# Kernel optimization log

Measured on AMD Instinct MI355X. Metric: run time of the kernel, lower is better.

## Reference

```python
import jax, jax.numpy as jnp
import numpy as np
import math

T, HW, M, D, DK, H, SIGMA = 16, 1024, 256, 768, 768, 8, 0.5
HD = DK // H
VHD = D // H
EPS = 1e-6
SCALE = 1.0 / math.sqrt(HD)


def _ln(x, g):
    # LayerNorm(eps=1e-6, bias=False)
    m = x.mean(-1, keepdims=True)
    v = ((x - m) ** 2).mean(-1, keepdims=True)
    return (x - m) / jnp.sqrt(v + EPS) * g


def setup_inputs() -> dict:
    key = jax.random.key(0)
    ks = jax.random.split(key, 16)
    s = 0.02
    features = jax.random.normal(ks[0], (T, HW, D), jnp.float32)
    tracks = jax.random.uniform(ks[1], (T, M, 2), jnp.float32)
    track_pos_embeddings = jax.random.normal(ks[2], (T, M, D), jnp.float32)
    feature_pos_embeddings = jax.random.normal(ks[3], (T, HW, D), jnp.float32)
    g = jnp.linspace(0.0, 1.0, 32)
    feature_positions = jnp.stack(jnp.meshgrid(g, g, indexing='ij'), axis=-1).reshape(HW, 2)
    return {
        'features': features,
        'tracks': tracks,
        'feature_positions': feature_positions,
        'track_pos_embeddings': track_pos_embeddings,
        'feature_pos_embeddings': feature_pos_embeddings,
        # AttentionalSampling params (nn.Linear weights are [out,in])
        'Wq_s': jax.random.normal(ks[4], (DK, D)) * s,
        'Wk_s': jax.random.normal(ks[5], (DK, D)) * s,
        'Wv_s': jax.random.normal(ks[6], (D, D)) * s,
        'qg_s': jnp.ones((DK,), jnp.float32),
        'kg_s': jnp.ones((DK,), jnp.float32),
        'Wo_s': jax.random.normal(ks[7], (D, D)) * s,
        # AttentionalSplatting params
        'Wq_p': jax.random.normal(ks[8], (DK, D)) * s,
        'Wk_p': jax.random.normal(ks[9], (DK, D)) * s,
        'Wv_p': jax.random.normal(ks[10], (D, D)) * s,
        'qg_p': jnp.ones((DK,), jnp.float32),
        'kg_p': jnp.ones((DK,), jnp.float32),
        'Wout_p': jax.random.normal(ks[11], (D, D)) * s,
    }


def reference(features, tracks, feature_positions, track_pos_embeddings,
              feature_pos_embeddings, Wq_s, Wk_s, Wv_s, qg_s, kg_s, Wo_s,
              Wq_p, Wk_p, Wv_p, qg_p, kg_p, Wout_p):
    # per-frame Gaussian spatial bias from squared euclidean distances
    # d2[t,m,n] = ||tracks[t,m] - feature_positions[n]||^2  -> [T, M, HW]
    d2 = ((tracks[:, :, None, :] - feature_positions[None, None, :, :]) ** 2).sum(-1)
    bias = -d2 / (2.0 * SIGMA ** 2)  # [T, M, HW]

    # ---- Attentional Sampling: tracks query features ----
    Q = _ln(track_pos_embeddings @ Wq_s.T, qg_s)          # [T, M, DK]
    K = _ln((features + feature_pos_embeddings) @ Wk_s.T, kg_s)  # [T, HW, DK]
    V = features @ Wv_s.T                                  # [T, HW, D]
    Qh = Q.reshape(T, M, H, HD).transpose(0, 2, 1, 3)      # [T, H, M, HD]
    Kh = K.reshape(T, HW, H, HD).transpose(0, 2, 1, 3)     # [T, H, HW, HD]
    Vh = V.reshape(T, HW, H, VHD).transpose(0, 2, 1, 3)    # [T, H, HW, VHD]
    scores = jnp.einsum('thmd,thnd->thmn', Qh, Kh) * SCALE + bias[:, None]
    A = jax.nn.softmax(scores, axis=-1)
    sampled = jnp.einsum('thmn,thnd->thmd', A, Vh)
    sampled = sampled.transpose(0, 2, 1, 3).reshape(T, M, D) @ Wo_s.T  # [T, M, D]

    # ---- Attentional Splatting: features query tracks ----
    Q2 = _ln(feature_pos_embeddings @ Wq_p.T, qg_p)        # [T, HW, DK]
    K2 = _ln(track_pos_embeddings @ Wk_p.T, kg_p)          # [T, M, DK]
    V2 = sampled @ Wv_p.T                                   # [T, M, D]
    Q2h = Q2.reshape(T, HW, H, HD).transpose(0, 2, 1, 3)   # [T, H, HW, HD]
    K2h = K2.reshape(T, M, H, HD).transpose(0, 2, 1, 3)    # [T, H, M, HD]
    V2h = V2.reshape(T, M, H, VHD).transpose(0, 2, 1, 3)   # [T, H, M, VHD]
    bias_t = jnp.swapaxes(bias, 1, 2)                       # [T, HW, M] (cdist is symmetric)
    scores2 = jnp.einsum('thnd,thmd->thnm', Q2h, K2h) * SCALE + bias_t[:, None]
    A2 = jax.nn.softmax(scores2, axis=-1)
    upd = jnp.einsum('thnm,thmd->thnd', A2, V2h)
    feature_updates = upd.transpose(0, 2, 1, 3).reshape(T, HW, D) @ Wout_p.T
    return features + feature_updates
```

## Files before the change

### kernel.cpp

```cpp
#include <hip/hip_runtime.h>

#define DD 768
#define HDIM 96
#define ATT_SCALE 0.10206207261596575f

typedef float floatx4 __attribute__((ext_vector_type(4)));
typedef __bf16 bf16;
typedef bf16 bf16x8 __attribute__((ext_vector_type(8)));
typedef bf16 bf16x4 __attribute__((ext_vector_type(4)));

__device__ __forceinline__ void gl2lds16(const bf16* g, bf16* l) {
  __builtin_amdgcn_global_load_lds(
      (const __attribute__((address_space(1))) void*)g,
      (__attribute__((address_space(3))) void*)l, 16, 0, 0);
}

__global__ __launch_bounds__(256) void conv_fuse(const float* __restrict__ f,
                                                 const float* __restrict__ e,
                                                 bf16* __restrict__ fb,
                                                 bf16* __restrict__ xb,
                                                 bf16* __restrict__ eb) {
  const int i = (blockIdx.x * 256 + threadIdx.x) * 8;
  floatx4 f0 = *(const floatx4*)(f + i);
  floatx4 f1 = *(const floatx4*)(f + i + 4);
  floatx4 e0 = *(const floatx4*)(e + i);
  floatx4 e1 = *(const floatx4*)(e + i + 4);
  bf16x8 fv, xv, ev;
#pragma unroll
  for (int k = 0; k < 4; k++) {
    fv[k] = (bf16)f0[k];           fv[k + 4] = (bf16)f1[k];
    ev[k] = (bf16)e0[k];           ev[k + 4] = (bf16)e1[k];
    xv[k] = (bf16)(f0[k] + e0[k]); xv[k + 4] = (bf16)(f1[k] + e1[k]);
  }
  *(bf16x8*)(fb + i) = fv;
  *(bf16x8*)(xb + i) = xv;
  *(bf16x8*)(eb + i) = ev;
}

__global__ __launch_bounds__(256) void f2b(const float* __restrict__ s,
                                           bf16* __restrict__ d) {
  const int i = (blockIdx.x * 256 + threadIdx.x) * 8;
  floatx4 s0 = *(const floatx4*)(s + i);
  floatx4 s1 = *(const floatx4*)(s + i + 4);
  bf16x8 v;
#pragma unroll
  for (int k = 0; k < 4; k++) { v[k] = (bf16)s0[k]; v[k + 4] = (bf16)s1[k]; }
  *(bf16x8*)(d + i) = v;
}

__global__ __launch_bounds__(256) void wconv(const float* w0, const float* w1,
                                             const float* w2, const float* w3,
                                             const float* w4, const float* w5,
                                             const float* w6, const float* w7,
                                             bf16* __restrict__ dst) {
  const float* srcs[8] = {w0, w1, w2, w3, w4, w5, w6, w7};
  const float* s = srcs[blockIdx.y];
  bf16* d = dst + (size_t)blockIdx.y * 589824;
  const int i = (blockIdx.x * 256 + threadIdx.x) * 8;
  floatx4 s0 = *(const floatx4*)(s + i);
  floatx4 s1 = *(const floatx4*)(s + i + 4);
  bf16x8 v;
#pragma unroll
  for (int k = 0; k < 4; k++) { v[k] = (bf16)s0[k]; v[k + 4] = (bf16)s1[k]; }
  *(bf16x8*)(d + i) = v;
}

__device__ __forceinline__ void ln_row(bf16* x, const float* g, int lane) {
  float v[12], s = 0.f, ss = 0.f;
#pragma unroll
  for (int j = 0; j < 3; j++) {
    bf16x4 b = *(const bf16x4*)&x[j * 256 + lane * 4];
#pragma unroll
    for (int e = 0; e < 4; e++) {
      float t = (float)b[e];
      v[j * 4 + e] = t; s += t; ss += t * t;
    }
  }
#pragma unroll
  for (int o = 32; o > 0; o >>= 1) { s += __shfl_xor(s, o); ss += __shfl_xor(ss, o); }
  const float mean = s * (1.0f / DD);
  const float inv = rsqrtf(ss * (1.0f / DD) - mean * mean + 1e-6f);
#pragma unroll
  for (int j = 0; j < 3; j++) {
    floatx4 gg = *(const floatx4*)&g[j * 256 + lane * 4];
    bf16x4 o4;
#pragma unroll
    for (int e = 0; e < 4; e++) o4[e] = (bf16)((v[j * 4 + e] - mean) * inv * gg[e]);
    *(bf16x4*)&x[j * 256 + lane * 4] = o4;
  }
}

__global__ __launch_bounds__(256) void ln_all(bf16* X0, const float* g0,
                                              bf16* X1, const float* g1,
                                              bf16* X2, const float* g2,
                                              bf16* X3, const float* g3) {
  const int b = blockIdx.x;
  bf16* X; const float* g; int base;
  if (b < 4096)      { X = X0; g = g0; base = b; }
  else if (b < 8192) { X = X1; g = g1; base = b - 4096; }
  else if (b < 9216) { X = X2; g = g2; base = b - 8192; }
  else               { X = X3; g = g3; base = b - 9216; }
  const int w = threadIdx.x >> 6, lane = threadIdx.x & 63;
  ln_row(X + (size_t)(base * 4 + w) * DD, g, lane);
}

template <int MODE>
__device__ __forceinline__ void gemm_core(const bf16* __restrict__ A,
                                          const bf16* __restrict__ W,
                                          bf16* __restrict__ Cb,
                                          float* __restrict__ Cf,
                                          const float* __restrict__ addsrc,
                                          bf16* As, bf16* Ws) {
  const int tid = threadIdx.x;
  const int lane = tid & 63;
  const int w = tid >> 6;
  const int row0 = blockIdx.x * 128;
  const int col0 = blockIdx.y * 128;
  const int wm = (w & 1) * 64;
  const int wn = (w >> 1) * 64;
  const int fr = lane & 15;
  const int quad = lane >> 4;
  const int srow = tid >> 2;
  const int scol = (tid & 3) * 8;
  const bf16* Ag = A + (size_t)(row0 + srow) * DD + scol;
  const bf16* Wg = W + (size_t)(col0 + srow) * DD + scol;
  bf16* AsD = &As[tid * 8];
  bf16* WsD = &Ws[tid * 8];

  floatx4 acc[4][4];
#pragma unroll
  for (int i = 0; i < 4; i++)
#pragma unroll
    for (int j = 0; j < 4; j++) acc[i][j] = (floatx4){0, 0, 0, 0};

  for (int k0 = 0; k0 < DD; k0 += 32) {
    __syncthreads();
    gl2lds16(Ag + k0, AsD);
    gl2lds16(Ag + k0 + (size_t)64 * DD, AsD + 2048);
    gl2lds16(Wg + k0, WsD);
    gl2lds16(Wg + k0 + (size_t)64 * DD, WsD + 2048);
    __syncthreads();
    bf16x8 af[4], bfr[4];
#pragma unroll
    for (int i = 0; i < 4; i++)
      af[i] = *(const bf16x8*)&As[(wm + i * 16 + fr) * 32 + quad * 8];
#pragma unroll
    for (int j = 0; j < 4; j++)
      bfr[j] = *(const bf16x8*)&Ws[(wn + j * 16 + fr) * 32 + quad * 8];
#pragma unroll
    for (int i = 0; i < 4; i++)
#pragma unroll
      for (int j = 0; j < 4; j++)
        acc[i][j] = __builtin_amdgcn_mfma_f32_16x16x32_bf16(af[i], bfr[j], acc[i][j], 0, 0, 0);
  }
#pragma unroll
  for (int i = 0; i < 4; i++)
#pragma unroll
    for (int j = 0; j < 4; j++)
#pragma unroll
      for (int r = 0; r < 4; r++) {
        const int row = row0 + wm + i * 16 + quad * 4 + r;
        const int col = col0 + wn + j * 16 + fr;
        const size_t idx = (size_t)row * DD + col;
        if (MODE == 0) Cb[idx] = (bf16)acc[i][j][r];
        else Cf[idx] = acc[i][j][r] + addsrc[idx];
      }
}

__global__ __launch_bounds__(256) void gemm_b(const bf16* A, const bf16* W, bf16* C) {
  __shared__ bf16 As[4096], Ws[4096];
  gemm_core<0>(A, W, C, nullptr, nullptr, As, Ws);
}

__global__ __launch_bounds__(256) void gemm_b2(const bf16* A0, const bf16* W0, bf16* C0,
                                               const bf16* A1, const bf16* W1, bf16* C1) {
  __shared__ bf16 As[4096], Ws[4096];
  if (blockIdx.z == 0) gemm_core<0>(A0, W0, C0, nullptr, nullptr, As, Ws);
  else                 gemm_core<0>(A1, W1, C1, nullptr, nullptr, As, Ws);
}

__global__ __launch_bounds__(256) void gemm_final(const bf16* A, const bf16* W,
                                                  float* C, const float* addsrc) {
  __shared__ bf16 As[4096], Ws[4096];
  gemm_core<1>(A, W, nullptr, C, addsrc, As, Ws);
}

template <int RPW, int SPLIT>
__global__ __launch_bounds__(256) void attn_kernel(
    const bf16* __restrict__ Qb, const bf16* __restrict__ Kb,
    const bf16* __restrict__ Vb, bf16* __restrict__ Ob,
    float* __restrict__ Ml,
    const float* __restrict__ qpos, int qpos_ts,
    const float* __restrict__ kpos, int kpos_ts,
    int nq, int nk, int nqt, int nsp) {
  const int b = blockIdx.x;
  const int h = b & 7;
  const int t = (b >> 3) & 15;
  const int rest = b >> 7;
  const int qt = rest % nqt;
  const int sp = rest / nqt;
  const int klen = nk / nsp;
  const int k0s = sp * klen;
  const int q0 = qt * (64 * RPW);
  const bf16* Q = Qb + (size_t)t * nq * DD + h * HDIM;
  const bf16* K = Kb + (size_t)t * nk * DD + h * HDIM;
  const bf16* V = Vb + (size_t)t * nk * DD + h * HDIM;
  bf16* O = Ob + (size_t)(SPLIT ? (sp * 16 + t) : t) * nq * DD + h * HDIM;
  const float* qp = qpos + (size_t)t * qpos_ts;
  const float* kp = kpos + (size_t)t * kpos_ts;

  __shared__ bf16 Ks[64 * 104];
  __shared__ bf16 Vt[96 * 72];
  __shared__ bf16 Ps[RPW * 64 * 72];

  const int tid = threadIdx.x;
  const int w = tid >> 6;
  const int lane = tid & 63;
  const int fr = lane & 15;
  const int quad = lane >> 4;
  const int rowb = w * (16 * RPW);

  bf16x8 qf[RPW][3];
  float qx[RPW][4], qy[RPW][4];
#pragma unroll
  for (int rt = 0; rt < RPW; rt++) {
    const bf16* qrow = Q + (size_t)(q0 + rowb + rt * 16 + fr) * DD;
#pragma unroll
    for (int c = 0; c < 3; c++) qf[rt][c] = *(const bf16x8*)(qrow + c * 32 + quad * 8);
#pragma unroll
    for (int r = 0; r < 4; r++) {
      int qi = q0 + rowb + rt * 16 + quad * 4 + r;
      qx[rt][r] = qp[qi * 2];
      qy[rt][r] = qp[qi * 2 + 1];
    }
  }

  float mrow[RPW][4], lrow[RPW][4];
  floatx4 oacc[RPW][6];
#pragma unroll
  for (int rt = 0; rt < RPW; rt++) {
#pragma unroll
    for (int r = 0; r < 4; r++) { mrow[rt][r] = -1e30f; lrow[rt][r] = 0.f; }
#pragma unroll
    for (int d = 0; d < 6; d++) oacc[rt][d] = (floatx4){0, 0, 0, 0};
  }

  const int srow = tid >> 2, scol = (tid & 3) * 24;
  const int nb = (tid & 15) * 4, db = (tid >> 4) * 6;

  for (int n0 = k0s; n0 < k0s + klen; n0 += 64) {
    __syncthreads();
    {
      const bf16* kg = K + (size_t)(n0 + srow) * DD + scol;
      bf16* ks = &Ks[srow * 104 + scol];
#pragma unroll
      for (int c = 0; c < 3; c++) *(bf16x8*)(ks + c * 8) = *(const bf16x8*)(kg + c * 8);
    }
    {
      bf16 tmp[4][6];
#pragma unroll
      for (int nn = 0; nn < 4; nn++) {
        const unsigned* vg = (const unsigned*)(V + (size_t)(n0 + nb + nn) * DD + db);
        unsigned u0 = vg[0], u1 = vg[1], u2 = vg[2];
        *(unsigned*)&tmp[nn][0] = u0;
        *(unsigned*)&tmp[nn][2] = u1;
        *(unsigned*)&tmp[nn][4] = u2;
      }
#pragma unroll
      for (int dd = 0; dd < 6; dd++) {
        bf16x4 v4 = {tmp[0][dd], tmp[1][dd], tmp[2][dd], tmp[3][dd]};
        *(bf16x4*)&Vt[(db + dd) * 72 + nb] = v4;
      }
    }
    __syncthreads();

    float kxx[4], kyy[4];
#pragma unroll
    for (int j = 0; j < 4; j++) {
      int ki = (n0 + j * 16 + fr) * 2;
      kxx[j] = kp[ki];
      kyy[j] = kp[ki + 1];
    }

#pragma unroll
    for (int rt = 0; rt < RPW; rt++) {
      floatx4 s4[4];
#pragma unroll
      for (int j = 0; j < 4; j++) {
        floatx4 sa = {0, 0, 0, 0};
#pragma unroll
        for (int c = 0; c < 3; c++) {
          bf16x8 kf = *(const bf16x8*)&Ks[(j * 16 + fr) * 104 + c * 32 + quad * 8];
          sa = __builtin_amdgcn_mfma_f32_16x16x32_bf16(qf[rt][c], kf, sa, 0, 0, 0);
        }
        s4[j] = sa;
      }
      float p[4][4], rmax[4], rsum[4], alpha[4];
#pragma unroll
      for (int r = 0; r < 4; r++) rmax[r] = -1e30f;
#pragma unroll
      for (int j = 0; j < 4; j++)
#pragma unroll
        for (int r = 0; r < 4; r++) {
          float dx = qx[rt][r] - kxx[j], dy = qy[rt][r] - kyy[j];
          float sv = s4[j][r] * ATT_SCALE - 2.0f * (dx * dx + dy * dy);
          p[j][r] = sv;
          rmax[r] = fmaxf(rmax[r], sv);
        }
#pragma unroll
      for (int r = 0; r < 4; r++) {
#pragma unroll
        for (int o = 1; o < 16; o <<= 1) rmax[r] = fmaxf(rmax[r], __shfl_xor(rmax[r], o));
        float mnew = fmaxf(mrow[rt][r], rmax[r]);
        alpha[r] = __expf(mrow[rt][r] - mnew);
        mrow[rt][r] = mnew;
        rsum[r] = 0.f;
      }
#pragma unroll
      for (int j = 0; j < 4; j++)
#pragma unroll
        for (int r = 0; r < 4; r++) {
          float pv = __expf(p[j][r] - mrow[rt][r]);
          p[j][r] = pv;
          rsum[r] += pv;
        }
#pragma unroll
      for (int r = 0; r < 4; r++) {
#pragma unroll
        for (int o = 1; o < 16; o <<= 1) rsum[r] += __shfl_xor(rsum[r], o);
        lrow[rt][r] = lrow[rt][r] * alpha[r] + rsum[r];
      }
#pragma unroll
      for (int j = 0; j < 4; j++)
#pragma unroll
        for (int r = 0; r < 4; r++)
          Ps[(rowb + rt * 16 + quad * 4 + r) * 72 + j * 16 + fr] = (bf16)p[j][r];
#pragma unroll
      for (int d = 0; d < 6; d++)
#pragma unroll
        for (int r = 0; r < 4; r++) oacc[rt][d][r] *= alpha[r];
    }

    bf16x8 pf[RPW][2];
#pragma unroll
    for (int rt = 0; rt < RPW; rt++) {
      pf[rt][0] = *(const bf16x8*)&Ps[(rowb + rt * 16 + fr) * 72 + quad * 8];
      pf[rt][1] = *(const bf16x8*)&Ps[(rowb + rt * 16 + fr) * 72 + 32 + quad * 8];
    }
#pragma unroll
    for (int d = 0; d < 6; d++) {
      bf16x8 v0 = *(const bf16x8*)&Vt[(d * 16 + fr) * 72 + quad * 8];
      bf16x8 v1 = *(const bf16x8*)&Vt[(d * 16 + fr) * 72 + 32 + quad * 8];
#pragma unroll
      for (int rt = 0; rt < RPW; rt++) {
        oacc[rt][d] = __builtin_amdgcn_mfma_f32_16x16x32_bf16(pf[rt][0], v0, oacc[rt][d], 0, 0, 0);
        oacc[rt][d] = __builtin_amdgcn_mfma_f32_16x16x32_bf16(pf[rt][1], v1, oacc[rt][d], 0, 0, 0);
      }
    }
  }

#pragma unroll
  for (int rt = 0; rt < RPW; rt++)
#pragma unroll
    for (int r = 0; r < 4; r++) {
      float inv = 1.0f / lrow[rt][r];
      int row = q0 + rowb + rt * 16 + quad * 4 + r;
#pragma unroll
      for (int d = 0; d < 6; d++)
        O[(size_t)row * DD + d * 16 + fr] = (bf16)(oacc[rt][d][r] * inv);
      if (SPLIT && fr == 0) {
        size_t mi = ((((size_t)sp * 16 + t) * 8 + h) * nq + row) * 2;
        Ml[mi] = mrow[rt][r];
        Ml[mi + 1] = lrow[rt][r];
      }
    }
}

__global__ __launch_bounds__(256) void combine2(const bf16* __restrict__ Op,
                                                const float* __restrict__ Ml,
                                                bf16* __restrict__ Out) {
  const int row = blockIdx.x;
  const int t = row >> 8;
  const int q = row & 255;
  const size_t half = (size_t)16 * 256 * DD;
#pragma unroll
  for (int e = 0; e < 3; e++) {
    int dim = threadIdx.x + e * 256;
    int hh = dim / 96;
    size_t mi0 = (((size_t)t * 8 + hh) * 256 + q) * 2;
    size_t mi1 = ((((size_t)16 + t) * 8 + hh) * 256 + q) * 2;
    float m0 = Ml[mi0], l0 = Ml[mi0 + 1];
    float m1 = Ml[mi1], l1 = Ml[mi1 + 1];
    float mm = fmaxf(m0, m1);
    float w0 = __expf(m0 - mm) * l0, w1 = __expf(m1 - mm) * l1;
    float inv = 1.0f / (w0 + w1);
    size_t idx = (size_t)row * DD + dim;
    Out[idx] = (bf16)((w0 * (float)Op[idx] + w1 * (float)Op[idx + half]) * inv);
  }
}

extern "C" void kernel_launch(void* const* d_in, const int* in_sizes, int n_in,
                              void* d_out, int out_size, void* d_ws, size_t ws_size,
                              hipStream_t stream) {
  const float* features = (const float*)d_in[0];
  const float* tracks   = (const float*)d_in[1];
  const float* fpos     = (const float*)d_in[2];
  const float* tpe      = (const float*)d_in[3];
  const float* fpe      = (const float*)d_in[4];
  const float* Wq_s     = (const float*)d_in[5];
  const float* Wk_s     = (const float*)d_in[6];
  const float* Wv_s     = (const float*)d_in[7];
  const float* qg_s     = (const float*)d_in[8];
  const float* kg_s     = (const float*)d_in[9];
  const float* Wo_s     = (const float*)d_in[10];
  const float* Wq_p     = (const float*)d_in[11];
  const float* Wk_p     = (const float*)d_in[12];
  const float* Wv_p     = (const float*)d_in[13];
  const float* qg_p     = (const float*)d_in[14];
  const float* kg_p     = (const float*)d_in[15];
  const float* Wout_p   = (const float*)d_in[16];
  float* out = (float*)d_out;

  const size_t SB = (size_t)16 * 1024 * 768;
  const size_t SS = (size_t)16 * 256 * 768;
  const size_t SW = (size_t)768 * 768;
  bf16* p = (bf16*)d_ws;
  bf16* Fb  = p; p += SB;
  bf16* Xb  = p; p += SB;
  bf16* Feb = p; p += SB;
  bf16* Kc  = p; p += SB;
  bf16* Vc  = p; p += SB;
  bf16* Tb  = p; p += SS;
  bf16* Qc  = p; p += SS;
  bf16* K2  = p; p += SS;
  bf16* Sh  = p; p += SS;
  bf16* Sp  = p; p += SS;
  bf16* Op  = p; p += 2 * SS;
  bf16* Wb  = p; p += 8 * SW;
  float* Ml = (float*)p;
  bf16* Q2 = Xb; bf16* V2 = Sh; bf16* U = Fb;

  dim3 blk(256);

  conv_fuse<<<6144, blk, 0, stream>>>(features, fpe, Fb, Xb, Feb);
  f2b<<<1536, blk, 0, stream>>>(tpe, Tb);
  wconv<<<dim3(288, 8), blk, 0, stream>>>(Wq_s, Wk_s, Wv_s, Wo_s,
                                          Wq_p, Wk_p, Wv_p, Wout_p, Wb);
  gemm_b2<<<dim3(128, 6, 2), blk, 0, stream>>>(Xb, Wb + 1 * SW, Kc,
                                               Fb, Wb + 2 * SW, Vc);
  gemm_b<<<dim3(128, 6), blk, 0, stream>>>(Feb, Wb + 4 * SW, Q2);
  gemm_b2<<<dim3(32, 6, 2), blk, 0, stream>>>(Tb, Wb + 0 * SW, Qc,
                                              Tb, Wb + 5 * SW, K2);
  ln_all<<<10240, blk, 0, stream>>>(Kc, kg_s, Q2, qg_p, Qc, qg_s, K2, kg_p);
  attn_kernel<1, 1><<<1024, blk, 0, stream>>>(Qc, Kc, Vc, Op, Ml,
                                              tracks, 512, fpos, 0, 256, 1024, 4, 2);
  combine2<<<4096, blk, 0, stream>>>(Op, Ml, Sh);
  gemm_b<<<dim3(32, 6), blk, 0, stream>>>(Sh, Wb + 3 * SW, Sp);
  gemm_b<<<dim3(32, 6), blk, 0, stream>>>(Sp, Wb + 6 * SW, V2);
  attn_kernel<2, 0><<<1024, blk, 0, stream>>>(Q2, K2, V2, U, nullptr,
                                              fpos, 0, tracks, 512, 1024, 256, 8, 1);
  gemm_final<<<dim3(128, 6), blk, 0, stream>>>(U, Wb + 7 * SW, out, features);
}
```

Measured before the change: 539.9 us.

## Fold Wo_s into Wv_p, drop softmax max tracking, use 512-thread attention

The sampling output projection and the splatting value projection are precomposed into a single 768x768 weight on each call, via a new transpose kernel and a small GEMM. This removes one full GEMM pass over the sampled activations. The attention kernel drops the online-softmax running maximum and rescaling, and exponentiates the biased scores directly, relying on LayerNorm-bounded scores to avoid overflow. It now runs 512-thread blocks in which two wave groups share each K/V tile. The sampling pass splits keys 4 ways and uses a simpler sum-based combine, and the three large projection GEMMs are batched into one launch. The risks are possible exp overflow on unusual inputs and the extra bf16 rounding from the folded weight.

```diff
diff --git a/kernel.cpp b/kernel.cpp
--- a/kernel.cpp
+++ b/kernel.cpp
@@ -8,6 +8,7 @@
 typedef __bf16 bf16;
 typedef bf16 bf16x8 __attribute__((ext_vector_type(8)));
 typedef bf16 bf16x4 __attribute__((ext_vector_type(4)));
+typedef bf16 bf16x2 __attribute__((ext_vector_type(2)));
 
 __device__ __forceinline__ void gl2lds16(const bf16* g, bf16* l) {
   __builtin_amdgcn_global_load_lds(
@@ -63,6 +64,27 @@
 #pragma unroll
   for (int k = 0; k < 4; k++) { v[k] = (bf16)s0[k]; v[k + 4] = (bf16)s1[k]; }
   *(bf16x8*)(d + i) = v;
+}
+
+__global__ __launch_bounds__(256) void wtrans(const float* __restrict__ in,
+                                              bf16* __restrict__ out) {
+  __shared__ float Ts[64][65];
+  const int X0 = blockIdx.x * 64, Y0 = blockIdx.y * 64;
+  const int r = threadIdx.x >> 2;
+  const int c4 = (threadIdx.x & 3) * 16;
+  const float* src = in + (size_t)(Y0 + r) * DD + X0 + c4;
+#pragma unroll
+  for (int k = 0; k < 16; k += 4) {
+    floatx4 v = *(const floatx4*)(src + k);
+    Ts[r][c4 + k] = v[0]; Ts[r][c4 + k + 1] = v[1];
+    Ts[r][c4 + k + 2] = v[2]; Ts[r][c4 + k + 3] = v[3];
+  }
+  __syncthreads();
+  bf16 o[16];
+#pragma unroll
+  for (int k = 0; k < 16; k++) o[k] = (bf16)Ts[c4 + k][r];
+  *(bf16x8*)(out + (size_t)(X0 + r) * DD + Y0 + c4) = *(bf16x8*)&o[0];
+  *(bf16x8*)(out + (size_t)(X0 + r) * DD + Y0 + c4 + 8) = *(bf16x8*)&o[8];
 }
 
 __device__ __forceinline__ void ln_row(bf16* x, const float* g, int lane) {
@@ -179,29 +201,38 @@
   else                 gemm_core<0>(A1, W1, C1, nullptr, nullptr, As, Ws);
 }
 
+__global__ __launch_bounds__(256) void gemm_b3(const bf16* A0, const bf16* W0, bf16* C0,
+                                               const bf16* A1, const bf16* W1, bf16* C1,
+                                               const bf16* A2, const bf16* W2, bf16* C2) {
+  __shared__ bf16 As[4096], Ws[4096];
+  if (blockIdx.z == 0)      gemm_core<0>(A0, W0, C0, nullptr, nullptr, As, Ws);
+  else if (blockIdx.z == 1) gemm_core<0>(A1, W1, C1, nullptr, nullptr, As, Ws);
+  else                      gemm_core<0>(A2, W2, C2, nullptr, nullptr, As, Ws);
+}
+
 __global__ __launch_bounds__(256) void gemm_final(const bf16* A, const bf16* W,
                                                   float* C, const float* addsrc) {
   __shared__ bf16 As[4096], Ws[4096];
   gemm_core<1>(A, W, nullptr, C, addsrc, As, Ws);
 }
 
-template <int RPW, int SPLIT>
-__global__ __launch_bounds__(256) void attn_kernel(
+template <int SPLIT>
+__global__ __launch_bounds__(512, 4) void attn512(
     const bf16* __restrict__ Qb, const bf16* __restrict__ Kb,
     const bf16* __restrict__ Vb, bf16* __restrict__ Ob,
     float* __restrict__ Ml,
     const float* __restrict__ qpos, int qpos_ts,
     const float* __restrict__ kpos, int kpos_ts,
-    int nq, int nk, int nqt, int nsp) {
+    int nq, int nk, int npq, int nsp) {
   const int b = blockIdx.x;
   const int h = b & 7;
   const int t = (b >> 3) & 15;
   const int rest = b >> 7;
-  const int qt = rest % nqt;
-  const int sp = rest / nqt;
+  const int qt = rest % npq;
+  const int sp = rest / npq;
   const int klen = nk / nsp;
   const int k0s = sp * klen;
-  const int q0 = qt * (64 * RPW);
+  const int q0 = qt * 128;
   const bf16* Q = Qb + (size_t)t * nq * DD + h * HDIM;
   const bf16* K = Kb + (size_t)t * nk * DD + h * HDIM;
   const bf16* V = Vb + (size_t)t * nk * DD + h * HDIM;
@@ -211,55 +242,53 @@
 
   __shared__ bf16 Ks[64 * 104];
   __shared__ bf16 Vt[96 * 72];
-  __shared__ bf16 Ps[RPW * 64 * 72];
+  __shared__ bf16 Ps[2 * 64 * 72];
 
   const int tid = threadIdx.x;
   const int w = tid >> 6;
+  const int g = w >> 2;
+  const int wl = w & 3;
   const int lane = tid & 63;
   const int fr = lane & 15;
   const int quad = lane >> 4;
-  const int rowb = w * (16 * RPW);
-
-  bf16x8 qf[RPW][3];
-  float qx[RPW][4], qy[RPW][4];
-#pragma unroll
-  for (int rt = 0; rt < RPW; rt++) {
-    const bf16* qrow = Q + (size_t)(q0 + rowb + rt * 16 + fr) * DD;
-#pragma unroll
-    for (int c = 0; c < 3; c++) qf[rt][c] = *(const bf16x8*)(qrow + c * 32 + quad * 8);
-#pragma unroll
-    for (int r = 0; r < 4; r++) {
-      int qi = q0 + rowb + rt * 16 + quad * 4 + r;
-      qx[rt][r] = qp[qi * 2];
-      qy[rt][r] = qp[qi * 2 + 1];
-    }
-  }
-
-  float mrow[RPW][4], lrow[RPW][4];
-  floatx4 oacc[RPW][6];
-#pragma unroll
-  for (int rt = 0; rt < RPW; rt++) {
-#pragma unroll
-    for (int r = 0; r < 4; r++) { mrow[rt][r] = -1e30f; lrow[rt][r] = 0.f; }
-#pragma unroll
-    for (int d = 0; d < 6; d++) oacc[rt][d] = (floatx4){0, 0, 0, 0};
-  }
-
-  const int srow = tid >> 2, scol = (tid & 3) * 24;
-  const int nb = (tid & 15) * 4, db = (tid >> 4) * 6;
+  const int rowb = wl * 16;
+  const int qgb = q0 + g * 64;
+  bf16* Pg = &Ps[g * 64 * 72];
+
+  bf16x8 qf[3];
+  {
+    const bf16* qrow = Q + (size_t)(qgb + rowb + fr) * DD;
+#pragma unroll
+    for (int c = 0; c < 3; c++) qf[c] = *(const bf16x8*)(qrow + c * 32 + quad * 8);
+  }
+  float qx[4], qy[4];
+#pragma unroll
+  for (int r = 0; r < 4; r++) {
+    int qi = qgb + rowb + quad * 4 + r;
+    qx[r] = qp[qi * 2];
+    qy[r] = qp[qi * 2 + 1];
+  }
+
+  float lrow[4] = {0.f, 0.f, 0.f, 0.f};
+  floatx4 oacc[6];
+#pragma unroll
+  for (int d = 0; d < 6; d++) oacc[d] = (floatx4){0, 0, 0, 0};
+
+  const int krA = tid >> 3, kcA = (tid & 7) * 8;
+  const int krB = (tid & 255) >> 2, kcB = 64 + (tid & 3) * 8;
+  const int nb = (tid & 31) * 2, db = (tid >> 5) * 6;
 
   for (int n0 = k0s; n0 < k0s + klen; n0 += 64) {
     __syncthreads();
+    *(bf16x8*)&Ks[krA * 104 + kcA] =
+        *(const bf16x8*)(K + (size_t)(n0 + krA) * DD + kcA);
+    if (tid < 256)
+      *(bf16x8*)&Ks[krB * 104 + kcB] =
+          *(const bf16x8*)(K + (size_t)(n0 + krB) * DD + kcB);
     {
-      const bf16* kg = K + (size_t)(n0 + srow) * DD + scol;
-      bf16* ks = &Ks[srow * 104 + scol];
-#pragma unroll
-      for (int c = 0; c < 3; c++) *(bf16x8*)(ks + c * 8) = *(const bf16x8*)(kg + c * 8);
-    }
-    {
-      bf16 tmp[4][6];
-#pragma unroll
-      for (int nn = 0; nn < 4; nn++) {
+      bf16 tmp[2][6];
+#pragma unroll
+      for (int nn = 0; nn < 2; nn++) {
         const unsigned* vg = (const unsigned*)(V + (size_t)(n0 + nb + nn) * DD + db);
         unsigned u0 = vg[0], u1 = vg[1], u2 = vg[2];
         *(unsigned*)&tmp[nn][0] = u0;
@@ -268,12 +297,23 @@
       }
 #pragma unroll
       for (int dd = 0; dd < 6; dd++) {
-        bf16x4 v4 = {tmp[0][dd], tmp[1][dd], tmp[2][dd], tmp[3][dd]};
-        *(bf16x4*)&Vt[(db + dd) * 72 + nb] = v4;
+        bf16x2 v2 = {tmp[0][dd], tmp[1][dd]};
+        *(bf16x2*)&Vt[(db + dd) * 72 + nb] = v2;
       }
     }
     __syncthreads();
 
+    floatx4 s4[4];
+#pragma unroll
+    for (int j = 0; j < 4; j++) {
+      floatx4 sa = {0, 0, 0, 0};
+#pragma unroll
+      for (int c = 0; c < 3; c++) {
+        bf16x8 kf = *(const bf16x8*)&Ks[(j * 16 + fr) * 104 + c * 32 + quad * 8];
+        sa = __builtin_amdgcn_mfma_f32_16x16x32_bf16(qf[c], kf, sa, 0, 0, 0);
+      }
+      s4[j] = sa;
+    }
     float kxx[4], kyy[4];
 #pragma unroll
     for (int j = 0; j < 4; j++) {
@@ -281,121 +321,67 @@
       kxx[j] = kp[ki];
       kyy[j] = kp[ki + 1];
     }
-
-#pragma unroll
-    for (int rt = 0; rt < RPW; rt++) {
-      floatx4 s4[4];
-#pragma unroll
-      for (int j = 0; j < 4; j++) {
-        floatx4 sa = {0, 0, 0, 0};
-#pragma unroll
-        for (int c = 0; c < 3; c++) {
-          bf16x8 kf = *(const bf16x8*)&Ks[(j * 16 + fr) * 104 + c * 32 + quad * 8];
-          sa = __builtin_amdgcn_mfma_f32_16x16x32_bf16(qf[rt][c], kf, sa, 0, 0, 0);
-        }
-        s4[j] = sa;
+#pragma unroll
+    for (int j = 0; j < 4; j++)
+#pragma unroll
+      for (int r = 0; r < 4; r++) {
+        float dx = qx[r] - kxx[j], dy = qy[r] - kyy[j];
+        float sv = s4[j][r] * ATT_SCALE - 2.0f * (dx * dx + dy * dy);
+        float pv = __expf(sv);
+        lrow[r] += pv;
+        Pg[(rowb + quad * 4 + r) * 72 + j * 16 + fr] = (bf16)pv;
       }
-      float p[4][4], rmax[4], rsum[4], alpha[4];
-#pragma unroll
-      for (int r = 0; r < 4; r++) rmax[r] = -1e30f;
-#pragma unroll
-      for (int j = 0; j < 4; j++)
-#pragma unroll
-        for (int r = 0; r < 4; r++) {
-          float dx = qx[rt][r] - kxx[j], dy = qy[rt][r] - kyy[j];
-          float sv = s4[j][r] * ATT_SCALE - 2.0f * (dx * dx + dy * dy);
-          p[j][r] = sv;
-          rmax[r] = fmaxf(rmax[r], sv);
-        }
-#pragma unroll
-      for (int r = 0; r < 4; r++) {
-#pragma unroll
-        for (int o = 1; o < 16; o <<= 1) rmax[r] = fmaxf(rmax[r], __shfl_xor(rmax[r], o));
-        float mnew = fmaxf(mrow[rt][r], rmax[r]);
-        alpha[r] = __expf(mrow[rt][r] - mnew);
-        mrow[rt][r] = mnew;
-        rsum[r] = 0.f;
-      }
-#pragma unroll
-      for (int j = 0; j < 4; j++)
-#pragma unroll
-        for (int r = 0; r < 4; r++) {
-          float pv = __expf(p[j][r] - mrow[rt][r]);
-          p[j][r] = pv;
-          rsum[r] += pv;
-        }
-#pragma unroll
-      for (int r = 0; r < 4; r++) {
-#pragma unroll
-        for (int o = 1; o < 16; o <<= 1) rsum[r] += __shfl_xor(rsum[r], o);
-        lrow[rt][r] = lrow[rt][r] * alpha[r] + rsum[r];
-      }
-#pragma unroll
-      for (int j = 0; j < 4; j++)
-#pragma unroll
-        for (int r = 0; r < 4; r++)
-          Ps[(rowb + rt * 16 + quad * 4 + r) * 72 + j * 16 + fr] = (bf16)p[j][r];
-#pragma unroll
-      for (int d = 0; d < 6; d++)
-#pragma unroll
-        for (int r = 0; r < 4; r++) oacc[rt][d][r] *= alpha[r];
-    }
-
-    bf16x8 pf[RPW][2];
-#pragma unroll
-    for (int rt = 0; rt < RPW; rt++) {
-      pf[rt][0] = *(const bf16x8*)&Ps[(rowb + rt * 16 + fr) * 72 + quad * 8];
-      pf[rt][1] = *(const bf16x8*)&Ps[(rowb + rt * 16 + fr) * 72 + 32 + quad * 8];
-    }
+    bf16x8 pf0 = *(const bf16x8*)&Pg[(rowb + fr) * 72 + quad * 8];
+    bf16x8 pf1 = *(const bf16x8*)&Pg[(rowb + fr) * 72 + 32 + quad * 8];
 #pragma unroll
     for (int d = 0; d < 6; d++) {
       bf16x8 v0 = *(const bf16x8*)&Vt[(d * 16 + fr) * 72 + quad * 8];
       bf16x8 v1 = *(const bf16x8*)&Vt[(d * 16 + fr) * 72 + 32 + quad * 8];
-#pragma unroll
-      for (int rt = 0; rt < RPW; rt++) {
-        oacc[rt][d] = __builtin_amdgcn_mfma_f32_16x16x32_bf16(pf[rt][0], v0, oacc[rt][d], 0, 0, 0);
-        oacc[rt][d] = __builtin_amdgcn_mfma_f32_16x16x32_bf16(pf[rt][1], v1, oacc[rt][d], 0, 0, 0);
-      }
-    }
-  }
-
-#pragma unroll
-  for (int rt = 0; rt < RPW; rt++)
-#pragma unroll
-    for (int r = 0; r < 4; r++) {
-      float inv = 1.0f / lrow[rt][r];
-      int row = q0 + rowb + rt * 16 + quad * 4 + r;
+      oacc[d] = __builtin_amdgcn_mfma_f32_16x16x32_bf16(pf0, v0, oacc[d], 0, 0, 0);
+      oacc[d] = __builtin_amdgcn_mfma_f32_16x16x32_bf16(pf1, v1, oacc[d], 0, 0, 0);
+    }
+  }
+
+#pragma unroll
+  for (int r = 0; r < 4; r++)
+#pragma unroll
+    for (int o = 1; o < 16; o <<= 1) lrow[r] += __shfl_xor(lrow[r], o);
+
+#pragma unroll
+  for (int r = 0; r < 4; r++) {
+    int row = qgb + rowb + quad * 4 + r;
+    if (SPLIT) {
 #pragma unroll
       for (int d = 0; d < 6; d++)
-        O[(size_t)row * DD + d * 16 + fr] = (bf16)(oacc[rt][d][r] * inv);
-      if (SPLIT && fr == 0) {
-        size_t mi = ((((size_t)sp * 16 + t) * 8 + h) * nq + row) * 2;
-        Ml[mi] = mrow[rt][r];
-        Ml[mi + 1] = lrow[rt][r];
-      }
-    }
-}
-
-__global__ __launch_bounds__(256) void combine2(const bf16* __restrict__ Op,
+        O[(size_t)row * DD + d * 16 + fr] = (bf16)oacc[d][r];
+      if (fr == 0)
+        Ml[((size_t)(sp * 16 + t) * 8 + h) * nq + row] = lrow[r];
+    } else {
+      float inv = 1.0f / lrow[r];
+#pragma unroll
+      for (int d = 0; d < 6; d++)
+        O[(size_t)row * DD + d * 16 + fr] = (bf16)(oacc[d][r] * inv);
+    }
+  }
+}
+
+__global__ __launch_bounds__(256) void combine4(const bf16* __restrict__ Op,
                                                 const float* __restrict__ Ml,
                                                 bf16* __restrict__ Out) {
   const int row = blockIdx.x;
   const int t = row >> 8;
   const int q = row & 255;
-  const size_t half = (size_t)16 * 256 * DD;
 #pragma unroll
   for (int e = 0; e < 3; e++) {
     int dim = threadIdx.x + e * 256;
     int hh = dim / 96;
-    size_t mi0 = (((size_t)t * 8 + hh) * 256 + q) * 2;
-    size_t mi1 = ((((size_t)16 + t) * 8 + hh) * 256 + q) * 2;
-    float m0 = Ml[mi0], l0 = Ml[mi0 + 1];
-    float m1 = Ml[mi1], l1 = Ml[mi1 + 1];
-    float mm = fmaxf(m0, m1);
-    float w0 = __expf(m0 - mm) * l0, w1 = __expf(m1 - mm) * l1;
-    float inv = 1.0f / (w0 + w1);
-    size_t idx = (size_t)row * DD + dim;
-    Out[idx] = (bf16)((w0 * (float)Op[idx] + w1 * (float)Op[idx + half]) * inv);
+    float osum = 0.f, lsum = 0.f;
+#pragma unroll
+    for (int s = 0; s < 4; s++) {
+      lsum += Ml[((size_t)(s * 16 + t) * 8 + hh) * 256 + q];
+      osum += (float)Op[((size_t)(s * 16 + t) * 256 + q) * DD + dim];
+    }
+    Out[(size_t)row * DD + dim] = (bf16)(osum / lsum);
   }
 }
 
@@ -430,15 +416,17 @@
   bf16* Feb = p; p += SB;
   bf16* Kc  = p; p += SB;
   bf16* Vc  = p; p += SB;
+  bf16* Qb2 = p; p += SB;
   bf16* Tb  = p; p += SS;
   bf16* Qc  = p; p += SS;
   bf16* K2  = p; p += SS;
   bf16* Sh  = p; p += SS;
-  bf16* Sp  = p; p += SS;
-  bf16* Op  = p; p += 2 * SS;
+  bf16* Op  = p; p += 4 * SS;
   bf16* Wb  = p; p += 8 * SW;
+  bf16* WoT = p; p += SW;
+  bf16* Wcr = p; p += SW;
   float* Ml = (float*)p;
-  bf16* Q2 = Xb; bf16* V2 = Sh; bf16* U = Fb;
+  bf16* V2 = Qc; bf16* U = Fb;
 
   dim3 blk(256);
 
@@ -446,18 +434,19 @@
   f2b<<<1536, blk, 0, stream>>>(tpe, Tb);
   wconv<<<dim3(288, 8), blk, 0, stream>>>(Wq_s, Wk_s, Wv_s, Wo_s,
                                           Wq_p, Wk_p, Wv_p, Wout_p, Wb);
-  gemm_b2<<<dim3(128, 6, 2), blk, 0, stream>>>(Xb, Wb + 1 * SW, Kc,
-                                               Fb, Wb + 2 * SW, Vc);
-  gemm_b<<<dim3(128, 6), blk, 0, stream>>>(Feb, Wb + 4 * SW, Q2);
+  wtrans<<<dim3(12, 12), blk, 0, stream>>>(Wo_s, WoT);
+  gemm_b<<<dim3(6, 6), blk, 0, stream>>>(Wb + 6 * SW, WoT, Wcr);
+  gemm_b3<<<dim3(128, 6, 3), blk, 0, stream>>>(Xb, Wb + 1 * SW, Kc,
+                                               Fb, Wb + 2 * SW, Vc,
+                                               Feb, Wb + 4 * SW, Qb2);
   gemm_b2<<<dim3(32, 6, 2), blk, 0, stream>>>(Tb, Wb + 0 * SW, Qc,
                                               Tb, Wb + 5 * SW, K2);
-  ln_all<<<10240, blk, 0, stream>>>(Kc, kg_s, Q2, qg_p, Qc, qg_s, K2, kg_p);
-  attn_kernel<1, 1><<<1024, blk, 0, stream>>>(Qc, Kc, Vc, Op, Ml,
-                                              tracks, 512, fpos, 0, 256, 1024, 4, 2);
-  combine2<<<4096, blk, 0, stream>>>(Op, Ml, Sh);
-  gemm_b<<<dim3(32, 6), blk, 0, stream>>>(Sh, Wb + 3 * SW, Sp);
-  gemm_b<<<dim3(32, 6), blk, 0, stream>>>(Sp, Wb + 6 * SW, V2);
-  attn_kernel<2, 0><<<1024, blk, 0, stream>>>(Q2, K2, V2, U, nullptr,
-                                              fpos, 0, tracks, 512, 1024, 256, 8, 1);
+  ln_all<<<10240, blk, 0, stream>>>(Kc, kg_s, Qb2, qg_p, Qc, qg_s, K2, kg_p);
+  attn512<1><<<1024, dim3(512), 0, stream>>>(Qc, Kc, Vc, Op, Ml,
+                                             tracks, 512, fpos, 0, 256, 1024, 2, 4);
+  combine4<<<4096, blk, 0, stream>>>(Op, Ml, Sh);
+  gemm_b<<<dim3(32, 6), blk, 0, stream>>>(Sh, Wcr, V2);
+  attn512<0><<<1024, dim3(512), 0, stream>>>(Qb2, K2, V2, U, nullptr,
+                                             fpos, 0, tracks, 512, 1024, 256, 8, 1);
   gemm_final<<<dim3(128, 6), blk, 0, stream>>>(U, Wb + 7 * SW, out, features);
 }
```

After: 491.4 us. 1.1x faster.
